# Performance work log

Hardware: AMD Instinct MI355X
Metric: run time of the kernel (lower is better)

Reference implementation:

```python
import jax, jax.numpy as jnp
import numpy as np

VOCAB = 100000
EDIM = 300
MUS = np.array([-0.9, -0.7, -0.5, -0.3, -0.1, 0.1, 0.3, 0.5, 0.7, 0.9, 1.0], dtype=np.float32)
SIGMAS = np.array([0.1] * 10 + [0.001], dtype=np.float32)


def setup_inputs() -> dict:
    key = jax.random.key(0)
    k1, k2, k3, k4, k5, k6 = jax.random.split(key, 6)
    B, Q, D = 128, 16, 1024
    doctoks = jax.random.randint(k1, (B, D), 0, VOCAB)
    querytoks = jax.random.randint(k2, (B, Q), 0, VOCAB)
    query_idf = jax.random.uniform(k3, (B, Q), dtype=jnp.float32)
    emb_table = jax.random.normal(k4, (VOCAB, EDIM), dtype=jnp.float32) * 0.1
    # pad token 0 -> zero embedding (padding_idx semantics)
    emb_table = emb_table.at[0].set(0.0)
    mus = jnp.asarray(MUS)
    sigmas = jnp.asarray(SIGMAS)
    K = mus.shape[0]
    fc_w = jax.random.normal(k5, (1, K), dtype=jnp.float32) * (1.0 / np.sqrt(K))
    fc_b = jax.random.normal(k6, (1,), dtype=jnp.float32) * 0.01
    return {"doctoks": doctoks, "querytoks": querytoks, "query_idf": query_idf,
            "emb_table": emb_table, "mus": mus, "sigmas": sigmas,
            "fc_w": fc_w, "fc_b": fc_b}


def reference(doctoks, querytoks, query_idf, emb_table, mus, sigmas, fc_w, fc_b):
    eps = 1e-9
    q_emb = emb_table[querytoks]                # [B,Q,E]
    d_emb = emb_table[doctoks]                  # [B,D,E]
    qn = q_emb / (jnp.linalg.norm(q_emb, axis=-1, keepdims=True) + eps)
    dn = d_emb / (jnp.linalg.norm(d_emb, axis=-1, keepdims=True) + eps)
    simmat = jnp.einsum('bqe,bde->bqd', qn, dn)  # cosine sim [B,Q,D]
    # zero out padded positions (token id 0)
    pad_mask = (querytoks != 0)[:, :, None] & (doctoks != 0)[:, None, :]
    simmat = jnp.where(pad_mask, simmat, 0.0)
    # RBF kernel bank broadcast at dim=1: [B,K,Q,D]
    diff = simmat[:, None, :, :] - mus[None, :, None, None]
    kernels = jnp.exp(-0.5 * diff * diff / (sigmas[None, :, None, None] ** 2))
    result = kernels.sum(axis=3)                 # [B,K,Q]
    mask = (simmat.sum(axis=2) != 0.0)[:, None, :]  # [B,1,Q] -> broadcasts over K
    mask = jnp.broadcast_to(mask, result.shape)
    result = jnp.where(mask, jnp.log(result + 1e-6), 0.0)
    result = result.sum(axis=2)                  # [B,K]
    scores = result @ fc_w.T + fc_b              # [B,1]
    return scores
```

## Files before the change

### kernel.cpp

```cpp
#include <hip/hip_runtime.h>

#define EDIM 300
#define NB   128
#define NQ   16
#define ND   1024
#define NK   11
#define BLOCK 128
#define MDOC  4
#define TDOCS 256
#define BLOCKS_PER_B 4
#define NPANEL 10
#define PPITCH 36
#define SIMP 260

__global__ __launch_bounds__(BLOCK) void knrm_main(
    const int*   __restrict__ dtoks,
    const int*   __restrict__ qtoks,
    const float* __restrict__ emb,
    const float* __restrict__ mus,
    const float* __restrict__ sigmas,
    float*       __restrict__ part) {
    __shared__ __align__(16) float qn_s[NQ * EDIM];
    __shared__ __align__(16) float panel[TDOCS * PPITCH];
    __shared__ int   dtok_s[TDOCS];
    __shared__ float rs_s[NQ];
    __shared__ __align__(16) float sim_t[NQ * SIMP];
    __shared__ float red_s[NK * NQ * 8];

    const int blk   = blockIdx.x;
    const int b     = blk >> 2;
    const int dbase = (blk & 3) * TDOCS;
    const int tid   = threadIdx.x;
    const int lane  = tid & 63;
    const int w     = tid >> 6;

    for (int i = tid; i < TDOCS; i += BLOCK) dtok_s[i] = dtoks[b * ND + dbase + i];
    for (int i = tid; i < NQ * EDIM; i += BLOCK) {
        int q = i / EDIM, e = i - q * EDIM;
        qn_s[i] = emb[(size_t)qtoks[b * NQ + q] * EDIM + e];
    }
    __syncthreads();
    {
        int q = tid >> 3, j = tid & 7;
        float ss = 0.f;
        for (int e = j; e < EDIM; e += 8) { float v = qn_s[q * EDIM + e]; ss += v * v; }
        ss += __shfl_xor(ss, 1, 64);
        ss += __shfl_xor(ss, 2, 64);
        ss += __shfl_xor(ss, 4, 64);
        if (j == 0) rs_s[q] = 1.0f / (sqrtf(ss) + 1e-9f);
    }
    __syncthreads();
    for (int i = tid; i < NQ * EDIM; i += BLOCK) qn_s[i] *= rs_s[i / EDIM];

    float sims[MDOC][8];
#pragma unroll
    for (int m = 0; m < MDOC; ++m)
#pragma unroll
        for (int qq = 0; qq < 8; ++qq) sims[m][qq] = 0.f;
    float ssq[MDOC] = {0.f, 0.f, 0.f, 0.f};

    const int s  = tid & 7;
    const int r0 = tid >> 3;

    for (int p = 0; p < NPANEL; ++p) {
        __syncthreads();
        if (p < 9 || s < 3) {
#pragma unroll
            for (int j = 0; j < 16; ++j) {
                int r = r0 + 16 * j;
                const float* src = emb + (size_t)dtok_s[r] * EDIM + p * 32 + s * 4;
                *(float4*)&panel[r * PPITCH + s * 4] = *(const float4*)src;
            }
        }
        __syncthreads();
        const int cmax = (p == 9) ? 3 : 8;
        for (int cc = 0; cc < cmax; ++cc) {
            float4 dv[MDOC];
#pragma unroll
            for (int m = 0; m < MDOC; ++m)
                dv[m] = *(const float4*)&panel[(lane + 64 * m) * PPITCH + cc * 4];
#pragma unroll
            for (int m = 0; m < MDOC; ++m)
                ssq[m] += dv[m].x*dv[m].x + dv[m].y*dv[m].y + dv[m].z*dv[m].z + dv[m].w*dv[m].w;
            const float* qb = qn_s + (size_t)w * 8 * EDIM + (p * 8 + cc) * 4;
#pragma unroll
            for (int qq = 0; qq < 8; ++qq) {
                float4 qv = *(const float4*)(qb + qq * EDIM);
#pragma unroll
                for (int m = 0; m < MDOC; ++m) {
                    sims[m][qq] += qv.x*dv[m].x + qv.y*dv[m].y + qv.z*dv[m].z + qv.w*dv[m].w;
                }
            }
        }
    }

#pragma unroll
    for (int m = 0; m < MDOC; ++m) {
        float rn = 1.0f / (sqrtf(ssq[m]) + 1e-9f);
#pragma unroll
        for (int qq = 0; qq < 8; ++qq)
            sim_t[(w * 8 + qq) * SIMP + lane + 64 * m] = sims[m][qq] * rn;
    }
    __syncthreads();

    {
        const int q = tid & 15;
        const int sl = tid >> 4;
        float mu[NK], cc2[NK], acc[NK];
#pragma unroll
        for (int k = 0; k < NK; ++k) {
            mu[k] = mus[k];
            float sg = sigmas[k];
            cc2[k] = -0.5f / (sg * sg);
            acc[k] = 0.f;
        }
        const float* row = sim_t + q * SIMP + sl * 32;
#pragma unroll
        for (int i = 0; i < 8; ++i) {
            float4 s4 = *(const float4*)(row + i * 4);
#pragma unroll
            for (int k = 0; k < NK; ++k) {
                float e0 = s4.x - mu[k], e1 = s4.y - mu[k];
                float e2 = s4.z - mu[k], e3 = s4.w - mu[k];
                acc[k] += __expf(cc2[k]*e0*e0) + __expf(cc2[k]*e1*e1)
                        + __expf(cc2[k]*e2*e2) + __expf(cc2[k]*e3*e3);
            }
        }
#pragma unroll
        for (int k = 0; k < NK; ++k) red_s[(k * NQ + q) * 8 + sl] = acc[k];
    }
    __syncthreads();

    for (int t = tid; t < NK * NQ; t += BLOCK) {
        float r = 0.f;
#pragma unroll
        for (int j = 0; j < 8; ++j) r += red_s[t * 8 + j];
        part[blk * (NK * NQ) + t] = r;
    }
}

__global__ void knrm_final(const float* __restrict__ part,
                           const int*   __restrict__ qtoks,
                           const float* __restrict__ fc_w,
                           const float* __restrict__ fc_b,
                           float*       __restrict__ out) {
    __shared__ float red[NK * NQ];
    __shared__ float ks[NK];
    int b = blockIdx.x;
    int t = threadIdx.x;
    if (t < NK * NQ) {
        int q = t & 15;
        float r = 0.f;
        for (int j = 0; j < BLOCKS_PER_B; ++j)
            r += part[(b * BLOCKS_PER_B + j) * (NK * NQ) + t];
        red[t] = (qtoks[b * NQ + q] != 0) ? logf(r + 1e-6f) : 0.f;
    }
    __syncthreads();
    if (t < NK) {
        float s = 0.f;
        for (int q = 0; q < NQ; ++q) s += red[t * NQ + q];
        ks[t] = s * fc_w[t];
    }
    __syncthreads();
    if (t == 0) {
        float s = fc_b[0];
        for (int k = 0; k < NK; ++k) s += ks[k];
        out[b] = s;
    }
}

extern "C" void kernel_launch(void* const* d_in, const int* in_sizes, int n_in,
                              void* d_out, int out_size, void* d_ws, size_t ws_size,
                              hipStream_t stream) {
    const int*   doctoks   = (const int*)  d_in[0];
    const int*   querytoks = (const int*)  d_in[1];
    const float* emb       = (const float*)d_in[3];
    const float* mus       = (const float*)d_in[4];
    const float* sigmas    = (const float*)d_in[5];
    const float* fc_w      = (const float*)d_in[6];
    const float* fc_b      = (const float*)d_in[7];
    float* out = (float*)d_out;

    float* part = (float*)d_ws;

    knrm_main<<<NB * BLOCKS_PER_B, BLOCK, 0, stream>>>(doctoks, querytoks, emb,
                                                       mus, sigmas, part);
    knrm_final<<<NB, 192, 0, stream>>>(part, querytoks, fc_w, fc_b, out);
}
```

Before: 222.3 us.

## Prefetch next document embedding panel into registers while computing current panel

Document embedding panels are now loaded from global memory into registers (16 float4 per thread) two panels ahead and written to shared memory after the current panel's compute, so global loads overlap the dot-product loop. The first panel load also overlaps query normalization. Query embedding loads and the normalization pass are vectorized to float4. The extra 64 registers per thread may reduce occupancy.

```diff
diff --git a/kernel.cpp b/kernel.cpp
--- a/kernel.cpp
+++ b/kernel.cpp
@@ -35,11 +35,36 @@
     const int w     = tid >> 6;
 
     for (int i = tid; i < TDOCS; i += BLOCK) dtok_s[i] = dtoks[b * ND + dbase + i];
-    for (int i = tid; i < NQ * EDIM; i += BLOCK) {
-        int q = i / EDIM, e = i - q * EDIM;
-        qn_s[i] = emb[(size_t)qtoks[b * NQ + q] * EDIM + e];
-    }
-    __syncthreads();
+    for (int i = tid; i < NQ * (EDIM / 4); i += BLOCK) {
+        int q = i / (EDIM / 4), e4 = i - q * (EDIM / 4);
+        ((float4*)qn_s)[i] =
+            *(const float4*)(emb + (size_t)qtoks[b * NQ + q] * EDIM + e4 * 4);
+    }
+    __syncthreads();
+
+    const int s  = tid & 7;
+    const int r0 = tid >> 3;
+    float4 pf[16];
+
+    auto pf_load = [&](int p) {
+        if (p < 9 || s < 3) {
+#pragma unroll
+            for (int j = 0; j < 16; ++j) {
+                const float* src =
+                    emb + (size_t)dtok_s[r0 + 16 * j] * EDIM + p * 32 + s * 4;
+                pf[j] = *(const float4*)src;
+            }
+        }
+    };
+    auto pf_write = [&](int p) {
+        if (p < 9 || s < 3) {
+#pragma unroll
+            for (int j = 0; j < 16; ++j)
+                *(float4*)&panel[(r0 + 16 * j) * PPITCH + s * 4] = pf[j];
+        }
+    };
+
+    pf_load(0);
     {
         int q = tid >> 3, j = tid & 7;
         float ss = 0.f;
@@ -50,7 +75,15 @@
         if (j == 0) rs_s[q] = 1.0f / (sqrtf(ss) + 1e-9f);
     }
     __syncthreads();
-    for (int i = tid; i < NQ * EDIM; i += BLOCK) qn_s[i] *= rs_s[i / EDIM];
+    for (int i = tid; i < NQ * (EDIM / 4); i += BLOCK) {
+        float4 v = ((float4*)qn_s)[i];
+        float r = rs_s[i / (EDIM / 4)];
+        v.x *= r; v.y *= r; v.z *= r; v.w *= r;
+        ((float4*)qn_s)[i] = v;
+    }
+    pf_write(0);
+    pf_load(1);
+    __syncthreads();
 
     float sims[MDOC][8];
 #pragma unroll
@@ -59,20 +92,7 @@
         for (int qq = 0; qq < 8; ++qq) sims[m][qq] = 0.f;
     float ssq[MDOC] = {0.f, 0.f, 0.f, 0.f};
 
-    const int s  = tid & 7;
-    const int r0 = tid >> 3;
-
     for (int p = 0; p < NPANEL; ++p) {
-        __syncthreads();
-        if (p < 9 || s < 3) {
-#pragma unroll
-            for (int j = 0; j < 16; ++j) {
-                int r = r0 + 16 * j;
-                const float* src = emb + (size_t)dtok_s[r] * EDIM + p * 32 + s * 4;
-                *(float4*)&panel[r * PPITCH + s * 4] = *(const float4*)src;
-            }
-        }
-        __syncthreads();
         const int cmax = (p == 9) ? 3 : 8;
         for (int cc = 0; cc < cmax; ++cc) {
             float4 dv[MDOC];
@@ -91,6 +111,12 @@
                     sims[m][qq] += qv.x*dv[m].x + qv.y*dv[m].y + qv.z*dv[m].z + qv.w*dv[m].w;
                 }
             }
+        }
+        __syncthreads();
+        if (p < 9) {
+            pf_write(p + 1);
+            if (p < 8) pf_load(p + 2);
+            __syncthreads();
         }
     }
 
```

Result: slower. 273.9 us (+23.2%).

## Register-prefetch next embedding panel to overlap gathers with dot-product compute

Applied to the files above, without the earlier changes.

Each thread now keeps 16 float4 registers holding the next panel of gathered document embeddings, loading panel p+2 while panel p is computed, and writing p+1 to shared memory after the compute loop. The query embedding load and normalization are vectorized to float4, and the first prefetch is issued before query normalization to hide its latency. Row pointers are precomputed once. This adds 64 registers per thread and sets launch_bounds min-blocks to 1, which may reduce occupancy.

```diff
diff --git a/kernel.cpp b/kernel.cpp
--- a/kernel.cpp
+++ b/kernel.cpp
@@ -13,7 +13,18 @@
 #define PPITCH 36
 #define SIMP 260
 
-__global__ __launch_bounds__(BLOCK) void knrm_main(
+
+#define PF_L(j)  pf##j = *(const float4*)(rp##j + pp * 32)
+#define PF_LOAD(p) do { const int pp = (p); if (pp < 9 || s < 3) { \
+    PF_L(0);  PF_L(1);  PF_L(2);  PF_L(3);  PF_L(4);  PF_L(5);  PF_L(6);  PF_L(7); \
+    PF_L(8);  PF_L(9);  PF_L(10); PF_L(11); PF_L(12); PF_L(13); PF_L(14); PF_L(15); } } while (0)
+
+#define PF_S(j)  *(float4*)&panel[(r0 + 16 * (j)) * PPITCH + s * 4] = pf##j
+#define PF_WRITE(p) do { if ((p) < 9 || s < 3) { \
+    PF_S(0);  PF_S(1);  PF_S(2);  PF_S(3);  PF_S(4);  PF_S(5);  PF_S(6);  PF_S(7); \
+    PF_S(8);  PF_S(9);  PF_S(10); PF_S(11); PF_S(12); PF_S(13); PF_S(14); PF_S(15); } } while (0)
+
+__global__ __launch_bounds__(BLOCK, 1) void knrm_main(
     const int*   __restrict__ dtoks,
     const int*   __restrict__ qtoks,
     const float* __restrict__ emb,
@@ -35,11 +46,37 @@
     const int w     = tid >> 6;
 
     for (int i = tid; i < TDOCS; i += BLOCK) dtok_s[i] = dtoks[b * ND + dbase + i];
-    for (int i = tid; i < NQ * EDIM; i += BLOCK) {
-        int q = i / EDIM, e = i - q * EDIM;
-        qn_s[i] = emb[(size_t)qtoks[b * NQ + q] * EDIM + e];
-    }
-    __syncthreads();
+    for (int i = tid; i < NQ * (EDIM / 4); i += BLOCK) {
+        int q = i / (EDIM / 4), e4 = i - q * (EDIM / 4);
+        ((float4*)qn_s)[i] =
+            *(const float4*)(emb + (size_t)qtoks[b * NQ + q] * EDIM + e4 * 4);
+    }
+    __syncthreads();
+
+    const int s  = tid & 7;
+    const int r0 = tid >> 3;
+
+    const float* rp0  = emb + (size_t)dtok_s[r0 +   0] * EDIM + s * 4;
+    const float* rp1  = emb + (size_t)dtok_s[r0 +  16] * EDIM + s * 4;
+    const float* rp2  = emb + (size_t)dtok_s[r0 +  32] * EDIM + s * 4;
+    const float* rp3  = emb + (size_t)dtok_s[r0 +  48] * EDIM + s * 4;
+    const float* rp4  = emb + (size_t)dtok_s[r0 +  64] * EDIM + s * 4;
+    const float* rp5  = emb + (size_t)dtok_s[r0 +  80] * EDIM + s * 4;
+    const float* rp6  = emb + (size_t)dtok_s[r0 +  96] * EDIM + s * 4;
+    const float* rp7  = emb + (size_t)dtok_s[r0 + 112] * EDIM + s * 4;
+    const float* rp8  = emb + (size_t)dtok_s[r0 + 128] * EDIM + s * 4;
+    const float* rp9  = emb + (size_t)dtok_s[r0 + 144] * EDIM + s * 4;
+    const float* rp10 = emb + (size_t)dtok_s[r0 + 160] * EDIM + s * 4;
+    const float* rp11 = emb + (size_t)dtok_s[r0 + 176] * EDIM + s * 4;
+    const float* rp12 = emb + (size_t)dtok_s[r0 + 192] * EDIM + s * 4;
+    const float* rp13 = emb + (size_t)dtok_s[r0 + 208] * EDIM + s * 4;
+    const float* rp14 = emb + (size_t)dtok_s[r0 + 224] * EDIM + s * 4;
+    const float* rp15 = emb + (size_t)dtok_s[r0 + 240] * EDIM + s * 4;
+
+    float4 pf0, pf1, pf2, pf3, pf4, pf5, pf6, pf7,
+           pf8, pf9, pf10, pf11, pf12, pf13, pf14, pf15;
+
+    PF_LOAD(0);
     {
         int q = tid >> 3, j = tid & 7;
         float ss = 0.f;
@@ -50,7 +87,15 @@
         if (j == 0) rs_s[q] = 1.0f / (sqrtf(ss) + 1e-9f);
     }
     __syncthreads();
-    for (int i = tid; i < NQ * EDIM; i += BLOCK) qn_s[i] *= rs_s[i / EDIM];
+    for (int i = tid; i < NQ * (EDIM / 4); i += BLOCK) {
+        float4 v = ((float4*)qn_s)[i];
+        float r = rs_s[i / (EDIM / 4)];
+        v.x *= r; v.y *= r; v.z *= r; v.w *= r;
+        ((float4*)qn_s)[i] = v;
+    }
+    PF_WRITE(0);
+    PF_LOAD(1);
+    __syncthreads();
 
     float sims[MDOC][8];
 #pragma unroll
@@ -59,20 +104,7 @@
         for (int qq = 0; qq < 8; ++qq) sims[m][qq] = 0.f;
     float ssq[MDOC] = {0.f, 0.f, 0.f, 0.f};
 
-    const int s  = tid & 7;
-    const int r0 = tid >> 3;
-
     for (int p = 0; p < NPANEL; ++p) {
-        __syncthreads();
-        if (p < 9 || s < 3) {
-#pragma unroll
-            for (int j = 0; j < 16; ++j) {
-                int r = r0 + 16 * j;
-                const float* src = emb + (size_t)dtok_s[r] * EDIM + p * 32 + s * 4;
-                *(float4*)&panel[r * PPITCH + s * 4] = *(const float4*)src;
-            }
-        }
-        __syncthreads();
         const int cmax = (p == 9) ? 3 : 8;
         for (int cc = 0; cc < cmax; ++cc) {
             float4 dv[MDOC];
@@ -91,6 +123,12 @@
                     sims[m][qq] += qv.x*dv[m].x + qv.y*dv[m].y + qv.z*dv[m].z + qv.w*dv[m].w;
                 }
             }
+        }
+        __syncthreads();
+        if (p < 9) {
+            PF_WRITE(p + 1);
+            if (p < 8) PF_LOAD(p + 2);
+            __syncthreads();
         }
     }
 
```

Result: faster. 213.5 us (-4.0%).

## Stage doc embeddings via global_load_lds in 32-doc tiles with fused RBF accumulation

Applied to the files above, without the earlier changes.

Rewrites the main kernel to load document embeddings in whole 32-row tiles straight into LDS with async global_load_lds, instead of 32-column panels through registers. Each wave splits the embedding dimension across lane groups and reduces with shuffles. The RBF kernel accumulation is fused per tile, which drops the sim_t and red_s shared buffers. The block grows to 256 threads for more parallel work. Because staging of the next tile is issued only after the barrier that ends the current compute, overlap is limited, and the early-issued async loads depend on the compiler inserting correct waits.

```diff
diff --git a/kernel.cpp b/kernel.cpp
--- a/kernel.cpp
+++ b/kernel.cpp
@@ -5,15 +5,21 @@
 #define NQ   16
 #define ND   1024
 #define NK   11
-#define BLOCK 128
-#define MDOC  4
+#define BLOCK 256
 #define TDOCS 256
 #define BLOCKS_PER_B 4
-#define NPANEL 10
-#define PPITCH 36
-#define SIMP 260
-
-__global__ __launch_bounds__(BLOCK) void knrm_main(
+#define DTILE 32
+#define NTILE 8
+#define NF4   75
+
+
+__device__ __forceinline__ void gload16(const float* g, float* l) {
+    __builtin_amdgcn_global_load_lds(
+        (const __attribute__((address_space(1))) void*)g,
+        (__attribute__((address_space(3))) void*)l, 16, 0, 0);
+}
+
+__global__ __launch_bounds__(BLOCK, 2) void knrm_main(
     const int*   __restrict__ dtoks,
     const int*   __restrict__ qtoks,
     const float* __restrict__ emb,
@@ -21,11 +27,9 @@
     const float* __restrict__ sigmas,
     float*       __restrict__ part) {
     __shared__ __align__(16) float qn_s[NQ * EDIM];
-    __shared__ __align__(16) float panel[TDOCS * PPITCH];
+    __shared__ __align__(16) float dpan[DTILE * EDIM];
     __shared__ int   dtok_s[TDOCS];
     __shared__ float rs_s[NQ];
-    __shared__ __align__(16) float sim_t[NQ * SIMP];
-    __shared__ float red_s[NK * NQ * 8];
 
     const int blk   = blockIdx.x;
     const int b     = blk >> 2;
@@ -34,108 +38,134 @@
     const int lane  = tid & 63;
     const int w     = tid >> 6;
 
-    for (int i = tid; i < TDOCS; i += BLOCK) dtok_s[i] = dtoks[b * ND + dbase + i];
-    for (int i = tid; i < NQ * EDIM; i += BLOCK) {
-        int q = i / EDIM, e = i - q * EDIM;
-        qn_s[i] = emb[(size_t)qtoks[b * NQ + q] * EDIM + e];
-    }
-    __syncthreads();
+    dtok_s[tid] = dtoks[b * ND + dbase + tid];
+#pragma unroll
+    for (int i = 0; i < 5; ++i) {
+        if (i < 4 || lane < 44) {
+            int fi = w * 300 + i * 64 + lane;
+            int q = fi / NF4, e4 = fi - q * NF4;
+            gload16(emb + (size_t)qtoks[b * NQ + q] * EDIM + e4 * 4, qn_s + fi * 4);
+        }
+    }
+    __syncthreads();
+
+#define STAGE(tb) do {                                                         \
+    _Pragma("unroll")                                                          \
+    for (int i_ = 0; i_ < 10; ++i_) {                                          \
+        if (i_ < 9 || lane < 24) {                                             \
+            int fi_ = w * 600 + i_ * 64 + lane;                                \
+            int r_ = fi_ / NF4, e4_ = fi_ - r_ * NF4;                          \
+            gload16(emb + (size_t)dtok_s[(tb) * DTILE + r_] * EDIM + e4_ * 4,  \
+                    dpan + fi_ * 4);                                           \
+        }                                                                      \
+    } } while (0)
+
+    STAGE(0);
+
     {
-        int q = tid >> 3, j = tid & 7;
+        int q = tid >> 4, j = tid & 15;
         float ss = 0.f;
-        for (int e = j; e < EDIM; e += 8) { float v = qn_s[q * EDIM + e]; ss += v * v; }
+        for (int e = j; e < EDIM; e += 16) { float v = qn_s[q * EDIM + e]; ss += v * v; }
         ss += __shfl_xor(ss, 1, 64);
         ss += __shfl_xor(ss, 2, 64);
         ss += __shfl_xor(ss, 4, 64);
+        ss += __shfl_xor(ss, 8, 64);
         if (j == 0) rs_s[q] = 1.0f / (sqrtf(ss) + 1e-9f);
     }
     __syncthreads();
-    for (int i = tid; i < NQ * EDIM; i += BLOCK) qn_s[i] *= rs_s[i / EDIM];
-
-    float sims[MDOC][8];
-#pragma unroll
-    for (int m = 0; m < MDOC; ++m)
-#pragma unroll
-        for (int qq = 0; qq < 8; ++qq) sims[m][qq] = 0.f;
-    float ssq[MDOC] = {0.f, 0.f, 0.f, 0.f};
-
-    const int s  = tid & 7;
-    const int r0 = tid >> 3;
-
-    for (int p = 0; p < NPANEL; ++p) {
+    for (int i = tid; i < NQ * NF4; i += BLOCK) {
+        float4 v = ((float4*)qn_s)[i];
+        float r = rs_s[i / NF4];
+        v.x *= r; v.y *= r; v.z *= r; v.w *= r;
+        ((float4*)qn_s)[i] = v;
+    }
+
+    const int d    = lane & 15;
+    const int g    = lane >> 4;
+    const int e4lo = g * 19;
+
+    float mu[3], c2[3];
+#pragma unroll
+    for (int j = 0; j < 3; ++j) {
+        int kk = g * 3 + j; if (kk > NK - 1) kk = NK - 1;
+        mu[j] = mus[kk];
+        float sg = sigmas[kk];
+        c2[j] = -0.5f / (sg * sg);
+    }
+    float racc[12];
+#pragma unroll
+    for (int t = 0; t < 12; ++t) racc[t] = 0.f;
+
+    for (int tb = 0; tb < NTILE; ++tb) {
         __syncthreads();
-        if (p < 9 || s < 3) {
-#pragma unroll
-            for (int j = 0; j < 16; ++j) {
-                int r = r0 + 16 * j;
-                const float* src = emb + (size_t)dtok_s[r] * EDIM + p * 32 + s * 4;
-                *(float4*)&panel[r * PPITCH + s * 4] = *(const float4*)src;
+        float sv[2][4], ssq[2];
+#pragma unroll
+        for (int m = 0; m < 2; ++m) { ssq[m] = 0.f;
+#pragma unroll
+            for (int qq = 0; qq < 4; ++qq) sv[m][qq] = 0.f; }
+
+        const float* dr0 = dpan + d * EDIM;
+        const float* dr1 = dpan + (d + 16) * EDIM;
+        const float* qb  = qn_s + (w * 4) * EDIM;
+#pragma unroll
+        for (int i = 0; i < 19; ++i) {
+            int e4 = e4lo + i;
+            if (e4 < NF4) {
+                float4 a = *(const float4*)(dr0 + e4 * 4);
+                float4 c = *(const float4*)(dr1 + e4 * 4);
+                ssq[0] += a.x*a.x + a.y*a.y + a.z*a.z + a.w*a.w;
+                ssq[1] += c.x*c.x + c.y*c.y + c.z*c.z + c.w*c.w;
+#pragma unroll
+                for (int qq = 0; qq < 4; ++qq) {
+                    float4 qv = *(const float4*)(qb + qq * EDIM + e4 * 4);
+                    sv[0][qq] += qv.x*a.x + qv.y*a.y + qv.z*a.z + qv.w*a.w;
+                    sv[1][qq] += qv.x*c.x + qv.y*c.y + qv.z*c.z + qv.w*c.w;
+                }
+            }
+        }
+#pragma unroll
+        for (int m = 0; m < 2; ++m) {
+            ssq[m] += __shfl_xor(ssq[m], 16, 64);
+            ssq[m] += __shfl_xor(ssq[m], 32, 64);
+#pragma unroll
+            for (int qq = 0; qq < 4; ++qq) {
+                sv[m][qq] += __shfl_xor(sv[m][qq], 16, 64);
+                sv[m][qq] += __shfl_xor(sv[m][qq], 32, 64);
+            }
+        }
+        float rn0 = 1.0f / (sqrtf(ssq[0]) + 1e-9f);
+        float rn1 = 1.0f / (sqrtf(ssq[1]) + 1e-9f);
+#pragma unroll
+        for (int qq = 0; qq < 4; ++qq) {
+            float s0 = sv[0][qq] * rn0;
+            float s1 = sv[1][qq] * rn1;
+#pragma unroll
+            for (int j = 0; j < 3; ++j) {
+                float e0 = s0 - mu[j], e1 = s1 - mu[j];
+                racc[j * 4 + qq] += __expf(c2[j] * e0 * e0) + __expf(c2[j] * e1 * e1);
             }
         }
         __syncthreads();
-        const int cmax = (p == 9) ? 3 : 8;
-        for (int cc = 0; cc < cmax; ++cc) {
-            float4 dv[MDOC];
-#pragma unroll
-            for (int m = 0; m < MDOC; ++m)
-                dv[m] = *(const float4*)&panel[(lane + 64 * m) * PPITCH + cc * 4];
-#pragma unroll
-            for (int m = 0; m < MDOC; ++m)
-                ssq[m] += dv[m].x*dv[m].x + dv[m].y*dv[m].y + dv[m].z*dv[m].z + dv[m].w*dv[m].w;
-            const float* qb = qn_s + (size_t)w * 8 * EDIM + (p * 8 + cc) * 4;
-#pragma unroll
-            for (int qq = 0; qq < 8; ++qq) {
-                float4 qv = *(const float4*)(qb + qq * EDIM);
-#pragma unroll
-                for (int m = 0; m < MDOC; ++m) {
-                    sims[m][qq] += qv.x*dv[m].x + qv.y*dv[m].y + qv.z*dv[m].z + qv.w*dv[m].w;
-                }
-            }
-        }
-    }
-
-#pragma unroll
-    for (int m = 0; m < MDOC; ++m) {
-        float rn = 1.0f / (sqrtf(ssq[m]) + 1e-9f);
-#pragma unroll
-        for (int qq = 0; qq < 8; ++qq)
-            sim_t[(w * 8 + qq) * SIMP + lane + 64 * m] = sims[m][qq] * rn;
-    }
-    __syncthreads();
-
-    {
-        const int q = tid & 15;
-        const int sl = tid >> 4;
-        float mu[NK], cc2[NK], acc[NK];
-#pragma unroll
-        for (int k = 0; k < NK; ++k) {
-            mu[k] = mus[k];
-            float sg = sigmas[k];
-            cc2[k] = -0.5f / (sg * sg);
-            acc[k] = 0.f;
-        }
-        const float* row = sim_t + q * SIMP + sl * 32;
-#pragma unroll
-        for (int i = 0; i < 8; ++i) {
-            float4 s4 = *(const float4*)(row + i * 4);
-#pragma unroll
-            for (int k = 0; k < NK; ++k) {
-                float e0 = s4.x - mu[k], e1 = s4.y - mu[k];
-                float e2 = s4.z - mu[k], e3 = s4.w - mu[k];
-                acc[k] += __expf(cc2[k]*e0*e0) + __expf(cc2[k]*e1*e1)
-                        + __expf(cc2[k]*e2*e2) + __expf(cc2[k]*e3*e3);
-            }
-        }
-#pragma unroll
-        for (int k = 0; k < NK; ++k) red_s[(k * NQ + q) * 8 + sl] = acc[k];
-    }
-    __syncthreads();
-
-    for (int t = tid; t < NK * NQ; t += BLOCK) {
-        float r = 0.f;
-#pragma unroll
-        for (int j = 0; j < 8; ++j) r += red_s[t * 8 + j];
-        part[blk * (NK * NQ) + t] = r;
+        if (tb + 1 < NTILE) STAGE(tb + 1);
+    }
+
+#pragma unroll
+    for (int t = 0; t < 12; ++t) {
+        racc[t] += __shfl_xor(racc[t], 1, 64);
+        racc[t] += __shfl_xor(racc[t], 2, 64);
+        racc[t] += __shfl_xor(racc[t], 4, 64);
+        racc[t] += __shfl_xor(racc[t], 8, 64);
+    }
+    if ((lane & 15) == 0) {
+        const int kb = g * 3;
+#pragma unroll
+        for (int j = 0; j < 3; ++j) {
+            if (g < 3 || j < 2) {
+#pragma unroll
+                for (int qq = 0; qq < 4; ++qq)
+                    part[blk * (NK * NQ) + (kb + j) * NQ + (w * 4 + qq)] = racc[j * 4 + qq];
+            }
+        }
     }
 }
 
```

New measurement: 255.1 us. +14.7%, slower.
